# Performance work log

Measured on AMD Instinct MI355X. Metric: run time of the kernel, lower is better.

Reference implementation:

```python
import jax, jax.numpy as jnp
import numpy as np

Q, B, D, H, DH, FF = 1024, 8, 1024, 16, 64, 4096


def layer_norm(x, g, b, eps=1e-5):
    mu = jnp.mean(x, axis=-1, keepdims=True)
    var = jnp.mean(jnp.square(x - mu), axis=-1, keepdims=True)
    return (x - mu) * jax.lax.rsqrt(var + eps) * g + b


def rel_shift(x):
    # x: [q, k, b, h] -> Transformer-XL relative shift
    q, k, b, h = x.shape
    x = jnp.concatenate([jnp.zeros((q, 1, b, h), x.dtype), x], axis=1)
    x = x.reshape(k + 1, q, b, h)[1:].reshape(q, k, b, h)
    return x


def setup_inputs() -> dict:
    key = jax.random.key(0)
    ks = jax.random.split(key, 12)
    s = 0.02
    return {
        "x": jax.random.normal(ks[0], (Q, B, D), jnp.float32),
        "pos_emb": jax.random.normal(ks[1], (Q, 1, D), jnp.float32),
        "attn_mask": jnp.zeros((Q, Q), dtype=bool),
        "ln1_g": jnp.ones((D,), jnp.float32),
        "ln1_b": jnp.zeros((D,), jnp.float32),
        "qkv_w": jax.random.normal(ks[2], (D, 3 * D), jnp.float32) * s,
        "qkv_b": jnp.zeros((3 * D,), jnp.float32),
        "r_w": jax.random.normal(ks[3], (D, D), jnp.float32) * s,
        "r_w_bias": jax.random.normal(ks[4], (H, DH), jnp.float32) * s,
        "r_r_bias": jax.random.normal(ks[5], (H, DH), jnp.float32) * s,
        "o_w": jax.random.normal(ks[6], (D, D), jnp.float32) * s,
        "ln2_g": jnp.ones((D,), jnp.float32),
        "ln2_b": jnp.zeros((D,), jnp.float32),
        "ffn_w1": jax.random.normal(ks[7], (D, FF), jnp.float32) * s,
        "ffn_b1": jnp.zeros((FF,), jnp.float32),
        "ffn_w2": jax.random.normal(ks[8], (FF, D), jnp.float32) * s,
        "ffn_b2": jnp.zeros((D,), jnp.float32),
    }


def reference(x, pos_emb, attn_mask, ln1_g, ln1_b, qkv_w, qkv_b, r_w,
              r_w_bias, r_r_bias, o_w, ln2_g, ln2_b, ffn_w1, ffn_b1,
              ffn_w2, ffn_b2):
    # ---- pre-norm + relative multi-head attention (Transformer-XL) ----
    q_in = layer_norm(x, ln1_g, ln1_b)                      # [Q,B,D]
    heads = q_in @ qkv_w + qkv_b                             # [Q,B,3D]
    wq, wk, wv = jnp.split(heads, 3, axis=-1)
    wq = wq.reshape(Q, B, H, DH)
    wk = wk.reshape(Q, B, H, DH)
    wv = wv.reshape(Q, B, H, DH)
    rk = (pos_emb[:, 0] @ r_w).reshape(Q, H, DH)             # [R,H,DH]

    scale = 1.0 / jnp.sqrt(jnp.asarray(DH, x.dtype))
    AC = jnp.einsum('ibhd,jbhd->ijbh', wq + r_w_bias, wk)    # content score
    BD = rel_shift(jnp.einsum('ibhd,jhd->ijbh', wq + r_r_bias, rk))
    score = (AC + BD) * scale                                # [Q,K,B,H]
    score = jnp.where(attn_mask[:, :, None, None], -1e30, score)
    prob = jax.nn.softmax(score, axis=1)
    attn_vec = jnp.einsum('ijbh,jbhd->ibhd', prob, wv).reshape(Q, B, D)
    x = x + attn_vec @ o_w                                   # residual

    # ---- pre-norm + position-wise FFN ----
    y = layer_norm(x, ln2_g, ln2_b)
    ffn = jax.nn.relu(y @ ffn_w1 + ffn_b1) @ ffn_w2 + ffn_b2
    return x + ffn
```

## Files before the change

### kernel.cpp

```cpp
#include <hip/hip_runtime.h>
#include <hip/hip_bf16.h>

#define QL  1024
#define BB  8
#define DD  1024
#define HH  16
#define DHH 64
#define FFD 4096

typedef __bf16 bf16x8 __attribute__((ext_vector_type(8)));
typedef float f32x4 __attribute__((ext_vector_type(4)));

union pk4 { ushort4 u; __hip_bfloat16 h[4]; };
union U8 { bf16x8 v; ushort u[8]; uint4 q; };
union BH { __hip_bfloat16 h; ushort u; };

__device__ inline ushort f2bu(float f) { BH t; t.h = __float2bfloat16(f); return t.u; }
__device__ inline float bu2f(ushort u) { BH t; t.u = u; return __bfloat162float(t.h); }

__device__ __forceinline__ void gload_lds16(const void* g, void* l) {
    __builtin_amdgcn_global_load_lds(
        (const __attribute__((address_space(1))) void*)g,
        (__attribute__((address_space(3))) void*)l, 16, 0, 0);
}

__global__ __launch_bounds__(256) void ln_kernel(const float* __restrict__ x,
                                                 const float* __restrict__ g,
                                                 const float* __restrict__ bta,
                                                 __hip_bfloat16* __restrict__ out) {
    __shared__ float red[8];
    int row = blockIdx.x;
    int t = threadIdx.x;
    const float* xr = x + (size_t)row * DD;
    float4 v = reinterpret_cast<const float4*>(xr)[t];
    float s = v.x + v.y + v.z + v.w;
    #pragma unroll
    for (int o = 32; o > 0; o >>= 1) s += __shfl_down(s, o, 64);
    int wid = t >> 6, lane = t & 63;
    if (lane == 0) red[wid] = s;
    __syncthreads();
    if (t == 0) red[4] = (red[0] + red[1] + red[2] + red[3]) * (1.0f / DD);
    __syncthreads();
    float mu = red[4];
    float d0 = v.x - mu, d1 = v.y - mu, d2 = v.z - mu, d3 = v.w - mu;
    float s2 = d0 * d0 + d1 * d1 + d2 * d2 + d3 * d3;
    #pragma unroll
    for (int o = 32; o > 0; o >>= 1) s2 += __shfl_down(s2, o, 64);
    if (lane == 0) red[wid] = s2;
    __syncthreads();
    if (t == 0) red[5] = rsqrtf((red[0] + red[1] + red[2] + red[3]) * (1.0f / DD) + 1e-5f);
    __syncthreads();
    float rs = red[5];
    float4 gv = reinterpret_cast<const float4*>(g)[t];
    float4 bv = reinterpret_cast<const float4*>(bta)[t];
    pk4 p;
    p.h[0] = __float2bfloat16(d0 * rs * gv.x + bv.x);
    p.h[1] = __float2bfloat16(d1 * rs * gv.y + bv.y);
    p.h[2] = __float2bfloat16(d2 * rs * gv.z + bv.z);
    p.h[3] = __float2bfloat16(d3 * rs * gv.w + bv.w);
    *reinterpret_cast<ushort4*>(out + (size_t)row * DD + t * 4) = p.u;
}

__global__ __launch_bounds__(256) void econv_kernel(const float* __restrict__ in,
                                                    __hip_bfloat16* __restrict__ out,
                                                    int n4) {
    int i = blockIdx.x * 256 + threadIdx.x;
    if (i < n4) {
        float4 v = reinterpret_cast<const float4*>(in)[i];
        pk4 p;
        p.h[0] = __float2bfloat16(v.x);
        p.h[1] = __float2bfloat16(v.y);
        p.h[2] = __float2bfloat16(v.z);
        p.h[3] = __float2bfloat16(v.w);
        reinterpret_cast<ushort4*>(out)[i] = p.u;
    }
}

__global__ __launch_bounds__(256) void wconv_kernel(const float* __restrict__ in,
                                                    __hip_bfloat16* __restrict__ out,
                                                    int K, int N) {
    __shared__ float t[32][33];
    int n0 = blockIdx.x * 32, k0 = blockIdx.y * 32;
    int tx = threadIdx.x & 31, ty = threadIdx.x >> 5;
    #pragma unroll
    for (int r = ty; r < 32; r += 8)
        t[r][tx] = in[(size_t)(k0 + r) * N + n0 + tx];
    __syncthreads();
    #pragma unroll
    for (int r = ty; r < 32; r += 8)
        out[(size_t)(n0 + r) * K + k0 + tx] = __float2bfloat16(t[tx][r]);
}

template <int RELU, int BF16OUT>
__global__ __launch_bounds__(256) void gemm_bf16_kernel(
    const __hip_bfloat16* __restrict__ A,
    const __hip_bfloat16* __restrict__ Bt,
    const float* __restrict__ bias,
    const float* __restrict__ res,
    void* __restrict__ Cv,
    int M, int N, int K) {
    __shared__ ushort As[128 * 64];
    __shared__ ushort Bs[128 * 64];
    int tid = threadIdx.x;
    int nwg = gridDim.x;
    int lin = blockIdx.x;
    int xcd = lin & 7, loc = lin >> 3;
    int qq = nwg >> 3, rr8 = nwg & 7;
    int swz = (xcd < rr8 ? xcd * (qq + 1) : rr8 * (qq + 1) + (xcd - rr8) * qq) + loc;
    int gx = N >> 7;
    int n0 = (swz % gx) * 128, m0 = (swz / gx) * 128;

    int lane = tid & 63, wid = tid >> 6;
    int wr = wid >> 1, wc = wid & 1;
    int rl = lane & 15, g = lane >> 4;

    int rin = lane >> 3;
    int sslot = (lane & 7) ^ rin;
    int c0 = wid * 4;

    f32x4 acc[4][4];
    #pragma unroll
    for (int m = 0; m < 4; m++)
        #pragma unroll
        for (int n = 0; n < 4; n++) {
            acc[m][n][0] = 0.f; acc[m][n][1] = 0.f;
            acc[m][n][2] = 0.f; acc[m][n][3] = 0.f;
        }

    for (int kb = 0; kb < K; kb += 64) {
        __syncthreads();
        #pragma unroll
        for (int q = 0; q < 4; q++) {
            int c = c0 + q;
            int row = c * 8 + rin;
            gload_lds16(A  + (size_t)(m0 + row) * K + kb + sslot * 8, &As[c * 512 + lane * 8]);
            gload_lds16(Bt + (size_t)(n0 + row) * K + kb + sslot * 8, &Bs[c * 512 + lane * 8]);
        }
        __syncthreads();
        #pragma unroll
        for (int k0 = 0; k0 < 2; k0++) {
            bf16x8 af[4], bfg[4];
            #pragma unroll
            for (int m = 0; m < 4; m++) {
                int row = wr * 64 + m * 16 + rl;
                int sw = ((k0 * 4 + g) ^ (row & 7)) * 8;
                af[m] = *reinterpret_cast<const bf16x8*>(&As[row * 64 + sw]);
            }
            #pragma unroll
            for (int n = 0; n < 4; n++) {
                int row = wc * 64 + n * 16 + rl;
                int sw = ((k0 * 4 + g) ^ (row & 7)) * 8;
                bfg[n] = *reinterpret_cast<const bf16x8*>(&Bs[row * 64 + sw]);
            }
            #pragma unroll
            for (int m = 0; m < 4; m++)
                #pragma unroll
                for (int n = 0; n < 4; n++)
                    acc[m][n] = __builtin_amdgcn_mfma_f32_16x16x32_bf16(
                        af[m], bfg[n], acc[m][n], 0, 0, 0);
        }
    }

    int rq = g * 4;
    #pragma unroll
    for (int n = 0; n < 4; n++) {
        int col = n0 + wc * 64 + n * 16 + rl;
        float bv = bias ? bias[col] : 0.f;
        #pragma unroll
        for (int m = 0; m < 4; m++) {
            int rbase = m0 + wr * 64 + m * 16 + rq;
            #pragma unroll
            for (int i = 0; i < 4; i++) {
                int row = rbase + i;
                float v = acc[m][n][i] + bv;
                if (res) v += res[(size_t)row * N + col];
                if (RELU) v = fmaxf(v, 0.f);
                if (BF16OUT)
                    reinterpret_cast<__hip_bfloat16*>(Cv)[(size_t)row * N + col] =
                        __float2bfloat16(v);
                else
                    reinterpret_cast<float*>(Cv)[(size_t)row * N + col] = v;
            }
        }
    }
}

__global__ __launch_bounds__(256) void bdg_kernel(
    const __hip_bfloat16* __restrict__ heads,
    const __hip_bfloat16* __restrict__ rkbf,
    const float* __restrict__ rrb,
    __hip_bfloat16* __restrict__ bdg, int b0) {
    __shared__ ushort As[128][72];
    __shared__ ushort Bs[128][72];
    int tid = threadIdx.x;
    int m0 = blockIdx.y * 128, n0 = blockIdx.x * 128;
    int zi = blockIdx.z;
    int h = zi & 15, b = b0 + (zi >> 4);

    {
        int row = tid >> 1, half = tid & 1;
        const __hip_bfloat16* qs =
            heads + ((size_t)(m0 + row) * BB + b) * (3 * DD) + h * DHH + half * 32;
        const float* wb = rrb + h * DHH + half * 32;
        #pragma unroll
        for (int c = 0; c < 4; c++) {
            U8 t; t.q = *reinterpret_cast<const uint4*>(qs + c * 8);
            U8 o;
            #pragma unroll
            for (int k = 0; k < 8; k++) o.u[k] = f2bu(bu2f(t.u[k]) + wb[c * 8 + k]);
            *reinterpret_cast<uint4*>(&As[row][half * 32 + c * 8]) = o.q;
        }
        const __hip_bfloat16* rs =
            rkbf + (size_t)(n0 + row) * DD + h * DHH + half * 32;
        #pragma unroll
        for (int c = 0; c < 4; c++)
            *reinterpret_cast<uint4*>(&Bs[row][half * 32 + c * 8]) =
                *reinterpret_cast<const uint4*>(rs + c * 8);
    }
    __syncthreads();

    int lane = tid & 63, wid = tid >> 6;
    int wr = wid >> 1, wc = wid & 1;
    int rl = lane & 15, g = lane >> 4;

    f32x4 acc[4][4];
    #pragma unroll
    for (int m = 0; m < 4; m++)
        #pragma unroll
        for (int n = 0; n < 4; n++) {
            acc[m][n][0] = 0.f; acc[m][n][1] = 0.f;
            acc[m][n][2] = 0.f; acc[m][n][3] = 0.f;
        }
    #pragma unroll
    for (int k0 = 0; k0 < 2; k0++) {
        bf16x8 af[4], bf[4];
        #pragma unroll
        for (int m = 0; m < 4; m++)
            af[m] = *reinterpret_cast<const bf16x8*>(&As[wr * 64 + m * 16 + rl][k0 * 32 + g * 8]);
        #pragma unroll
        for (int n = 0; n < 4; n++)
            bf[n] = *reinterpret_cast<const bf16x8*>(&Bs[wc * 64 + n * 16 + rl][k0 * 32 + g * 8]);
        #pragma unroll
        for (int m = 0; m < 4; m++)
            #pragma unroll
            for (int n = 0; n < 4; n++)
                acc[m][n] = __builtin_amdgcn_mfma_f32_16x16x32_bf16(
                    af[m], bf[n], acc[m][n], 0, 0, 0);
    }

    __hip_bfloat16* base = bdg + (size_t)zi * QL * QL;
    #pragma unroll
    for (int m = 0; m < 4; m++)
        #pragma unroll
        for (int n = 0; n < 4; n++)
            #pragma unroll
            for (int r = 0; r < 4; r++) {
                int i_ = m0 + wr * 64 + m * 16 + g * 4 + r;
                int rr = n0 + wc * 64 + n * 16 + rl;
                int i, j;
                if (rr >= QL - 1 - i_) { i = i_; j = rr - (QL - 1) + i_; }
                else if (i_ > 0)       { i = i_ - 1; j = rr + i_ + 1; }
                else continue;
                int qt = i >> 4, g2 = (i >> 2) & 3, r2 = i & 3;
                int jt = j >> 4, l2 = j & 15;
                base[(((size_t)(qt * 64 + jt)) * 64 + g2 * 16 + l2) * 4 + r2] =
                    __float2bfloat16(acc[m][n][r]);
            }
}

__global__ __launch_bounds__(512, 4) void attn_kernel(
    const __hip_bfloat16* __restrict__ heads,
    const __hip_bfloat16* __restrict__ bdg,
    const float* __restrict__ rwb,
    __hip_bfloat16* __restrict__ av, int b0) {
    __shared__ ushort Ks[2][64][72];
    __shared__ ushort Vts[2][64][72];
    __shared__ ushort Plds[128][72];

    int tid = threadIdx.x;
    int w = tid >> 6, lane = tid & 63;
    int g = lane >> 4, l = lane & 15;
    int i0 = blockIdx.x * 128;
    int lb = blockIdx.y, h = blockIdx.z;
    int b = b0 + lb;
    const __hip_bfloat16* bdb = bdg + (size_t)(lb * HH + h) * QL * QL;
    int qt = (i0 >> 4) + w;

    bf16x8 qf[2];
    {
        int qrow = i0 + w * 16 + l;
        const __hip_bfloat16* qs =
            heads + ((size_t)qrow * BB + b) * (3 * DD) + h * DHH;
        #pragma unroll
        for (int k0 = 0; k0 < 2; k0++) {
            U8 t; t.q = *reinterpret_cast<const uint4*>(qs + k0 * 32 + g * 8);
            const float* wv = rwb + h * DHH + k0 * 32 + g * 8;
            U8 o;
            #pragma unroll
            for (int k = 0; k < 8; k++) o.u[k] = f2bu(bu2f(t.u[k]) + wv[k]);
            qf[k0] = o.v;
        }
    }

    float m_r[4], l_r[4];
    f32x4 o_acc[4];
    #pragma unroll
    for (int r = 0; r < 4; r++) { m_r[r] = -INFINITY; l_r[r] = 0.f; }
    #pragma unroll
    for (int dd = 0; dd < 4; dd++) {
        o_acc[dd][0] = 0.f; o_acc[dd][1] = 0.f;
        o_acc[dd][2] = 0.f; o_acc[dd][3] = 0.f;
    }

    int sr = tid >> 3, sc = tid & 7;
    for (int jt = 0; jt < 16; jt++) {
        int j0 = jt * 64;
        int cur = jt & 1;
        {
            const __hip_bfloat16* kb =
                heads + ((size_t)(j0 + sr) * BB + b) * (3 * DD) + DD + h * DHH + sc * 8;
            *reinterpret_cast<uint4*>(&Ks[cur][sr][sc * 8]) =
                *reinterpret_cast<const uint4*>(kb);
            U8 vv; vv.q = *reinterpret_cast<const uint4*>(kb + DD);
            #pragma unroll
            for (int k = 0; k < 8; k++) Vts[cur][sc * 8 + k][sr] = vv.u[k];
        }
        __syncthreads();

        f32x4 s[4];
        #pragma unroll
        for (int jj = 0; jj < 4; jj++) {
            bf16x8 kf0 = *reinterpret_cast<const bf16x8*>(&Ks[cur][jj * 16 + l][g * 8]);
            bf16x8 kf1 = *reinterpret_cast<const bf16x8*>(&Ks[cur][jj * 16 + l][32 + g * 8]);
            f32x4 t = {0.f, 0.f, 0.f, 0.f};
            t = __builtin_amdgcn_mfma_f32_16x16x32_bf16(qf[0], kf0, t, 0, 0, 0);
            t = __builtin_amdgcn_mfma_f32_16x16x32_bf16(qf[1], kf1, t, 0, 0, 0);
            s[jj] = t;
        }

        #pragma unroll
        for (int jj = 0; jj < 4; jj++) {
            int jtg = (j0 >> 4) + jj;
            pk4 bd;
            bd.u = *reinterpret_cast<const ushort4*>(
                bdb + (((size_t)(qt * 64 + jtg)) * 64 + lane) * 4);
            int gj = j0 + jj * 16 + l;
            #pragma unroll
            for (int r = 0; r < 4; r++) {
                int gi = i0 + w * 16 + g * 4 + r;
                float add = (gj == gi + 1) ? 0.f : __bfloat162float(bd.h[r]);
                s[jj][r] = (s[jj][r] + add) * 0.125f;
            }
        }

        float arow[4], mrow[4], psum[4];
        #pragma unroll
        for (int r = 0; r < 4; r++) {
            float mx = fmaxf(fmaxf(s[0][r], s[1][r]), fmaxf(s[2][r], s[3][r]));
            #pragma unroll
            for (int o = 1; o < 16; o <<= 1) mx = fmaxf(mx, __shfl_xor(mx, o, 64));
            float mn = fmaxf(m_r[r], mx);
            arow[r] = __expf(m_r[r] - mn);
            m_r[r] = mn; mrow[r] = mn; psum[r] = 0.f;
        }
        #pragma unroll
        for (int jj = 0; jj < 4; jj++)
            #pragma unroll
            for (int r = 0; r < 4; r++) {
                float pv = __expf(s[jj][r] - mrow[r]);
                psum[r] += pv;
                Plds[w * 16 + g * 4 + r][jj * 16 + l] = f2bu(pv);
            }
        #pragma unroll
        for (int r = 0; r < 4; r++) {
            float ps = psum[r];
            #pragma unroll
            for (int o = 1; o < 16; o <<= 1) ps += __shfl_xor(ps, o, 64);
            l_r[r] = l_r[r] * arow[r] + ps;
            #pragma unroll
            for (int dd = 0; dd < 4; dd++) o_acc[dd][r] *= arow[r];
        }

        #pragma unroll
        for (int jc = 0; jc < 2; jc++) {
            bf16x8 pf = *reinterpret_cast<const bf16x8*>(&Plds[w * 16 + l][jc * 32 + g * 8]);
            #pragma unroll
            for (int dd = 0; dd < 4; dd++) {
                bf16x8 vf = *reinterpret_cast<const bf16x8*>(&Vts[cur][dd * 16 + l][jc * 32 + g * 8]);
                o_acc[dd] = __builtin_amdgcn_mfma_f32_16x16x32_bf16(pf, vf, o_acc[dd], 0, 0, 0);
            }
        }
    }

    #pragma unroll
    for (int r = 0; r < 4; r++) {
        int gi = i0 + w * 16 + g * 4 + r;
        float inv = 1.0f / l_r[r];
        __hip_bfloat16* dst = av + ((size_t)gi * BB + b) * DD + h * DHH;
        #pragma unroll
        for (int dd = 0; dd < 4; dd++) {
            BH t; t.u = f2bu(o_acc[dd][r] * inv);
            dst[dd * 16 + l] = t.h;
        }
    }
}

extern "C" void kernel_launch(void* const* d_in, const int* in_sizes, int n_in,
                              void* d_out, int out_size, void* d_ws, size_t ws_size,
                              hipStream_t stream) {
    (void)in_sizes; (void)n_in; (void)out_size;
    const float* x        = (const float*)d_in[0];
    const float* pos_emb  = (const float*)d_in[1];
    const float* ln1_g    = (const float*)d_in[3];
    const float* ln1_b    = (const float*)d_in[4];
    const float* qkv_w    = (const float*)d_in[5];
    const float* qkv_b    = (const float*)d_in[6];
    const float* r_w      = (const float*)d_in[7];
    const float* r_w_bias = (const float*)d_in[8];
    const float* r_r_bias = (const float*)d_in[9];
    const float* o_w      = (const float*)d_in[10];
    const float* ln2_g    = (const float*)d_in[11];
    const float* ln2_b    = (const float*)d_in[12];
    const float* ffn_w1   = (const float*)d_in[13];
    const float* ffn_b1   = (const float*)d_in[14];
    const float* ffn_w2   = (const float*)d_in[15];
    const float* ffn_b2   = (const float*)d_in[16];
    float* out = (float*)d_out;

    char* p = (char*)d_ws;
    __hip_bfloat16* heads = (__hip_bfloat16*)p; p += (size_t)8192 * 3072 * 2;
    __hip_bfloat16* rkbf  = (__hip_bfloat16*)p; p += (size_t)1024 * 1024 * 2;
    __hip_bfloat16* abf   = (__hip_bfloat16*)p; p += (size_t)8192 * 1024 * 2;
    __hip_bfloat16* qkvwt = (__hip_bfloat16*)p; p += (size_t)3072 * 1024 * 2;
    __hip_bfloat16* owt   = (__hip_bfloat16*)p; p += (size_t)1024 * 1024 * 2;
    __hip_bfloat16* w1t   = (__hip_bfloat16*)p; p += (size_t)4096 * 1024 * 2;
    __hip_bfloat16* w2t   = (__hip_bfloat16*)p; p += (size_t)1024 * 4096 * 2;
    __hip_bfloat16* pebf  = (__hip_bfloat16*)p; p += (size_t)1024 * 1024 * 2;
    __hip_bfloat16* rwt   = (__hip_bfloat16*)p; p += (size_t)1024 * 1024 * 2;
    char* shared = p;
    __hip_bfloat16* bdg  = (__hip_bfloat16*)shared;
    __hip_bfloat16* f1bf = (__hip_bfloat16*)shared;

    size_t used = (size_t)(p - (char*)d_ws);
    size_t avail_b = ws_size > used ? ws_size - used : 0;

    size_t per_b = (size_t)HH * QL * QL * 2;
    int bb = 1;
    if (avail_b >= 8 * per_b) bb = 8;
    else if (avail_b >= 4 * per_b) bb = 4;
    else if (avail_b >= 2 * per_b) bb = 2;

    int chunk_rows = 2048;
    if (avail_b >= (size_t)8192 * 4096 * 2) chunk_rows = 8192;
    else if (avail_b >= (size_t)4096 * 4096 * 2) chunk_rows = 4096;
    int n_chunks = 8192 / chunk_rows;

    wconv_kernel<<<dim3(3072 / 32, 1024 / 32), 256, 0, stream>>>(qkv_w, qkvwt, 1024, 3072);
    wconv_kernel<<<dim3(1024 / 32, 1024 / 32), 256, 0, stream>>>(o_w, owt, 1024, 1024);
    wconv_kernel<<<dim3(4096 / 32, 1024 / 32), 256, 0, stream>>>(ffn_w1, w1t, 1024, 4096);
    wconv_kernel<<<dim3(1024 / 32, 4096 / 32), 256, 0, stream>>>(ffn_w2, w2t, 4096, 1024);
    wconv_kernel<<<dim3(1024 / 32, 1024 / 32), 256, 0, stream>>>(r_w, rwt, 1024, 1024);
    econv_kernel<<<dim3(1024), 256, 0, stream>>>(pos_emb, pebf, 1024 * 1024 / 4);
    ln_kernel<<<QL * BB, 256, 0, stream>>>(x, ln1_g, ln1_b, abf);
    gemm_bf16_kernel<0, 1><<<dim3(24 * 64), 256, 0, stream>>>(
        abf, qkvwt, qkv_b, nullptr, heads, 8192, 3072, 1024);
    gemm_bf16_kernel<0, 1><<<dim3(8 * 8), 256, 0, stream>>>(
        pebf, rwt, nullptr, nullptr, rkbf, 1024, 1024, 1024);
    for (int b0 = 0; b0 < BB; b0 += bb) {
        bdg_kernel<<<dim3(8, 8, bb * HH), 256, 0, stream>>>(
            heads, rkbf, r_r_bias, bdg, b0);
        attn_kernel<<<dim3(QL / 128, bb, HH), 512, 0, stream>>>(
            heads, bdg, r_w_bias, abf, b0);
    }
    gemm_bf16_kernel<0, 0><<<dim3(8 * 64), 256, 0, stream>>>(
        abf, owt, nullptr, x, out, 8192, 1024, 1024);
    ln_kernel<<<QL * BB, 256, 0, stream>>>(out, ln2_g, ln2_b, abf);
    for (int c = 0; c < n_chunks; c++) {
        const __hip_bfloat16* yc = abf + (size_t)c * chunk_rows * 1024;
        float* oc = out + (size_t)c * chunk_rows * 1024;
        gemm_bf16_kernel<1, 1><<<dim3((4096 / 128) * (chunk_rows / 128)), 256, 0, stream>>>(
            yc, w1t, ffn_b1, nullptr, f1bf, chunk_rows, 4096, 1024);
        gemm_bf16_kernel<0, 0><<<dim3((1024 / 128) * (chunk_rows / 128)), 256, 0, stream>>>(
            f1bf, w2t, ffn_b2, oc, oc, chunk_rows, 1024, 4096);
    }
}
```

Measured before the change: 827.3 us.

## Double-buffer LDS tiles in bf16 GEMM with async prefetch two stages ahead

Splits the GEMM's shared-memory A/B tiles into two buffers and issues global-to-LDS loads for tile kt+2 while computing on tile kt. Explicit vmcnt waits and raw barriers replace the two __syncthreads per iteration. The aim is to hide global load latency behind the MFMA work. In exchange it doubles LDS use to 64KB per block, which may reduce occupancy, and it depends on the vmcnt counts being exactly right.

```diff
diff --git a/kernel.cpp b/kernel.cpp
--- a/kernel.cpp
+++ b/kernel.cpp
@@ -99,8 +99,8 @@
     const float* __restrict__ res,
     void* __restrict__ Cv,
     int M, int N, int K) {
-    __shared__ ushort As[128 * 64];
-    __shared__ ushort Bs[128 * 64];
+    __shared__ ushort As[2][128 * 64];
+    __shared__ ushort Bs[2][128 * 64];
     int tid = threadIdx.x;
     int nwg = gridDim.x;
     int lin = blockIdx.x;
@@ -127,16 +127,28 @@
             acc[m][n][2] = 0.f; acc[m][n][3] = 0.f;
         }
 
-    for (int kb = 0; kb < K; kb += 64) {
-        __syncthreads();
-        #pragma unroll
-        for (int q = 0; q < 4; q++) {
-            int c = c0 + q;
-            int row = c * 8 + rin;
-            gload_lds16(A  + (size_t)(m0 + row) * K + kb + sslot * 8, &As[c * 512 + lane * 8]);
-            gload_lds16(Bt + (size_t)(n0 + row) * K + kb + sslot * 8, &Bs[c * 512 + lane * 8]);
-        }
-        __syncthreads();
+    #define STAGE(bf, kb)                                                          \
+        _Pragma("unroll")                                                          \
+        for (int q = 0; q < 4; q++) {                                              \
+            int c = c0 + q;                                                        \
+            int row = c * 8 + rin;                                                 \
+            gload_lds16(A  + (size_t)(m0 + row) * K + (kb) + sslot * 8,            \
+                        &As[bf][c * 512 + lane * 8]);                              \
+            gload_lds16(Bt + (size_t)(n0 + row) * K + (kb) + sslot * 8,            \
+                        &Bs[bf][c * 512 + lane * 8]);                              \
+        }
+
+    int NT = K >> 6;
+    STAGE(0, 0);
+    STAGE(1, 64);
+    asm volatile("s_waitcnt vmcnt(8)" ::: "memory");
+    __builtin_amdgcn_s_barrier();
+    __builtin_amdgcn_sched_barrier(0);
+
+    for (int kt = 0; kt < NT; kt++) {
+        int cur = kt & 1;
+        const ushort* Ab = As[cur];
+        const ushort* Bb = Bs[cur];
         #pragma unroll
         for (int k0 = 0; k0 < 2; k0++) {
             bf16x8 af[4], bfg[4];
@@ -144,13 +156,13 @@
             for (int m = 0; m < 4; m++) {
                 int row = wr * 64 + m * 16 + rl;
                 int sw = ((k0 * 4 + g) ^ (row & 7)) * 8;
-                af[m] = *reinterpret_cast<const bf16x8*>(&As[row * 64 + sw]);
+                af[m] = *reinterpret_cast<const bf16x8*>(&Ab[row * 64 + sw]);
             }
             #pragma unroll
             for (int n = 0; n < 4; n++) {
                 int row = wc * 64 + n * 16 + rl;
                 int sw = ((k0 * 4 + g) ^ (row & 7)) * 8;
-                bfg[n] = *reinterpret_cast<const bf16x8*>(&Bs[row * 64 + sw]);
+                bfg[n] = *reinterpret_cast<const bf16x8*>(&Bb[row * 64 + sw]);
             }
             #pragma unroll
             for (int m = 0; m < 4; m++)
@@ -159,7 +171,19 @@
                     acc[m][n] = __builtin_amdgcn_mfma_f32_16x16x32_bf16(
                         af[m], bfg[n], acc[m][n], 0, 0, 0);
         }
-    }
+        if (kt == NT - 1) break;
+        __builtin_amdgcn_sched_barrier(0);
+        __builtin_amdgcn_s_barrier();
+        if (kt + 2 < NT) {
+            STAGE(cur, (kt + 2) << 6);
+            asm volatile("s_waitcnt vmcnt(8)" ::: "memory");
+        } else {
+            asm volatile("s_waitcnt vmcnt(0)" ::: "memory");
+        }
+        __builtin_amdgcn_s_barrier();
+        __builtin_amdgcn_sched_barrier(0);
+    }
+    #undef STAGE
 
     int rq = g * 4;
     #pragma unroll
```

Measured after the change: 829.2 us. No clear change (+0.2%).
